# Optimization experiments

Hardware: AMD Instinct MI355X
Metric: run time of the kernel (lower is better)

## Reference

```python
import jax, jax.numpy as jnp
import numpy as np

ALPHA = 1.702
LIMIT = 7.0


def setup_inputs() -> dict:
    key = jax.random.key(0)
    ks = jax.random.split(key, 6)
    A, B, E, M, H = 1, 1, 8, 1024, 2048
    I2 = 4096  # 2 * intermediate_size, interleaved gate/up
    inter = I2 // 2
    return {
        "dispatched": jax.random.normal(ks[0], (A, B, E, M, H), dtype=jnp.float32),
        "w1": jax.random.normal(ks[1], (E, H, I2), dtype=jnp.float32) * 0.02,
        "w1_bias": jax.random.normal(ks[2], (E, I2), dtype=jnp.float32) * 0.02,
        "w2": jax.random.normal(ks[3], (E, inter, H), dtype=jnp.float32) * 0.02,
        "w2_bias": jax.random.normal(ks[4], (E, H), dtype=jnp.float32) * 0.02,
        "sparsity_remap": jax.random.randint(ks[5], (E,), 0, E, dtype=jnp.int32),
        "BD": 1,
        "S": 1024,
    }


def reference(dispatched, w1, w1_bias, w2, w2_bias, sparsity_remap, BD, S):
    # dispatched: [A, B, E, M, H]; w1: [E, H, 2I]; w2: [E, I, H]
    # tt.sparse_matmul == grouped per-expert GEMM; dense math is identical.
    A, Bt, E, M, H = dispatched.shape
    # fused gate+up projection: [A, B, E, M, 2I]
    gu = jnp.einsum("abemh,ehn->abemn", dispatched, w1) + w1_bias[None, None, :, None, :]
    # interleaved gate/up split (gpt_oss activation path)
    gate = gu[..., 0::2]
    up = gu[..., 1::2]
    gate = jnp.minimum(gate, LIMIT)
    up = jnp.clip(up, -LIMIT, LIMIT)
    glu = gate * jax.nn.sigmoid(gate * ALPHA)
    activated = (up + 1.0) * glu  # [A, B, E, M, I]
    inter = activated.shape[-1]
    activated = activated.reshape(A * Bt, E, M, inter)
    # down projection: [A*B, E, M, H]
    down = jnp.einsum("bemi,eih->bemh", activated, w2) + w2_bias[None, :, None, :]
    # permute(1,0,2,3) then untile to [E, 1, BD*S, H]
    out = jnp.transpose(down, (1, 0, 2, 3)).reshape(E, 1, BD * S, H)
    return out
```

## Files before the change

kernel.cpp:

```cpp
#include <hip/hip_runtime.h>
#include <hip/hip_bf16.h>
#include <cstdint>
#include <cstddef>

#define E_ 8
#define M_ 1024
#define H_ 2048
#define I2_ 4096
#define INTER_ 2048

typedef __attribute__((ext_vector_type(8))) __bf16 bf16x8;
typedef __attribute__((ext_vector_type(4))) float f32x4;

__device__ __forceinline__ unsigned short f2bf(float x) {
  union { float f; unsigned u; } v; v.f = x;
  unsigned r = v.u + 0x7fffu + ((v.u >> 16) & 1u);
  return (unsigned short)(r >> 16);
}

__global__ void k_cvt(const float* __restrict__ src, unsigned short* __restrict__ dst, int n4) {
  int i = blockIdx.x * blockDim.x + threadIdx.x;
  int stride = gridDim.x * blockDim.x;
  const float4* s4 = (const float4*)src;
  ushort4* d4 = (ushort4*)dst;
  for (; i < n4; i += stride) {
    float4 v = s4[i];
    ushort4 o;
    o.x = f2bf(v.x); o.y = f2bf(v.y); o.z = f2bf(v.z); o.w = f2bf(v.w);
    d4[i] = o;
  }
}

template<int REMAP>
__global__ __launch_bounds__(1024) void k_transpose(const float* __restrict__ src,
                                                    unsigned short* __restrict__ dst,
                                                    int Ks, int Ns) {
  __shared__ float t[32][65];
  int e = blockIdx.z;
  const float* s = src + (size_t)e * Ks * Ns;
  unsigned short* d = dst + (size_t)e * Ks * Ns;
  int k0 = blockIdx.x * 64;
  int n0 = blockIdx.y * 32;
  int tx = threadIdx.x, ty = threadIdx.y;
  t[tx][ty]      = s[(size_t)(k0 + ty) * Ns + n0 + tx];
  t[tx][ty + 32] = s[(size_t)(k0 + ty + 32) * Ns + n0 + tx];
  __syncthreads();
  int sl = REMAP ? (((ty & 15) << 1) | (ty >> 4)) : ty;
  unsigned short lo = f2bf(t[sl][2 * tx]);
  unsigned short hi = f2bf(t[sl][2 * tx + 1]);
  unsigned v = (unsigned)lo | ((unsigned)hi << 16);
  *(unsigned*)(d + (size_t)(n0 + ty) * Ks + k0 + 2 * tx) = v;
}

template<int ACT, int N, int K>
__global__ __launch_bounds__(256) void k_gemm(
    const unsigned short* __restrict__ A,
    const unsigned short* __restrict__ Bt,
    const float* __restrict__ bias,
    unsigned short* __restrict__ ActOut,
    float* __restrict__ Out)
{
  __shared__ unsigned short la[128 * 64];
  __shared__ unsigned short lb[128 * 64];
  const int tid = threadIdx.x;
  const int lane = tid & 63;
  const int wv = tid >> 6;
  const int wm = wv & 1, wn = wv >> 1;
  const int e = blockIdx.z;
  const int n0 = blockIdx.x * 128;
  const int m0 = blockIdx.y * 128;
  const unsigned short* Ae = A + (size_t)e * M_ * K + (size_t)m0 * K;
  const unsigned short* Be = Bt + (size_t)e * N * K + (size_t)n0 * K;

  const unsigned short* ga[4];
  const unsigned short* gb[4];
  int segb[4];
  #pragma unroll
  for (int t = 0; t < 4; ++t) {
    int s = (wv * 4 + t) * 64 + lane;
    int m = s >> 3;
    int j = (s & 7) ^ (m & 7);
    ga[t] = Ae + (size_t)m * K + j * 8;
    gb[t] = Be + (size_t)m * K + j * 8;
    segb[t] = (wv * 4 + t) * 1024;
  }

  const int c = lane & 15;
  const int q = lane >> 4;

  f32x4 acc[4][4];
  const f32x4 zero = {0.f, 0.f, 0.f, 0.f};
  #pragma unroll
  for (int i = 0; i < 4; ++i)
    #pragma unroll
    for (int j = 0; j < 4; ++j) acc[i][j] = zero;

  const int KT = K / 64;
  for (int kt = 0; kt < KT; ++kt) {
    #pragma unroll
    for (int t = 0; t < 4; ++t) {
      __builtin_amdgcn_global_load_lds(
          (const __attribute__((address_space(1))) void*)(const void*)(ga[t] + kt * 64),
          (__attribute__((address_space(3))) void*)(void*)((char*)la + segb[t]), 16, 0, 0);
      __builtin_amdgcn_global_load_lds(
          (const __attribute__((address_space(1))) void*)(const void*)(gb[t] + kt * 64),
          (__attribute__((address_space(3))) void*)(void*)((char*)lb + segb[t]), 16, 0, 0);
    }
    __syncthreads();
    #pragma unroll
    for (int ks = 0; ks < 2; ++ks) {
      bf16x8 av[4], bv[4];
      #pragma unroll
      for (int mi = 0; mi < 4; ++mi) {
        int row = wm * 64 + mi * 16 + c;
        int slot = row * 8 + ((ks * 4 + q) ^ (c & 7));
        av[mi] = *(const bf16x8*)(la + slot * 8);
      }
      #pragma unroll
      for (int ni = 0; ni < 4; ++ni) {
        int row = wn * 64 + ni * 16 + c;
        int slot = row * 8 + ((ks * 4 + q) ^ (c & 7));
        bv[ni] = *(const bf16x8*)(lb + slot * 8);
      }
      #pragma unroll
      for (int mi = 0; mi < 4; ++mi)
        #pragma unroll
        for (int ni = 0; ni < 4; ++ni)
          acc[mi][ni] = __builtin_amdgcn_mfma_f32_16x16x32_bf16(av[mi], bv[ni], acc[mi][ni], 0, 0, 0);
    }
    __syncthreads();
  }

  if (ACT) {
    unsigned short* ActE = ActOut + (size_t)e * M_ * (N / 2);
    const float* be = bias + (size_t)e * N;
    int colbase = n0 + wn * 64;
    #pragma unroll
    for (int p = 0; p < 2; ++p) {
      int rg = colbase + 32 * p + c;
      int norig = (rg & ~31) | (c << 1);
      float bg = be[norig];
      float bu = be[norig + 1];
      int acol = ((rg >> 5) << 4) + c;
      #pragma unroll
      for (int mi = 0; mi < 4; ++mi) {
        int rowb = m0 + wm * 64 + mi * 16 + q * 4;
        #pragma unroll
        for (int r = 0; r < 4; ++r) {
          float g = acc[mi][2 * p][r] + bg;
          float u = acc[mi][2 * p + 1][r] + bu;
          g = fminf(g, 7.0f);
          u = fminf(fmaxf(u, -7.0f), 7.0f);
          float glu = g / (1.0f + __expf(-1.702f * g));
          float a = (u + 1.0f) * glu;
          ActE[(size_t)(rowb + r) * (N / 2) + acol] = f2bf(a);
        }
      }
    }
  } else {
    float* OutE = Out + (size_t)e * M_ * N;
    const float* be = bias + (size_t)e * N;
    #pragma unroll
    for (int ni = 0; ni < 4; ++ni) {
      int col = n0 + wn * 64 + ni * 16 + c;
      float bb = be[col];
      #pragma unroll
      for (int mi = 0; mi < 4; ++mi) {
        int rowb = m0 + wm * 64 + mi * 16 + q * 4;
        #pragma unroll
        for (int r = 0; r < 4; ++r)
          OutE[(size_t)(rowb + r) * N + col] = acc[mi][ni][r] + bb;
      }
    }
  }
}

__global__ __launch_bounds__(256) void k_naive(const float* __restrict__ disp,
    const float* __restrict__ w1, const float* __restrict__ w1b,
    const float* __restrict__ w2, const float* __restrict__ w2b,
    float* __restrict__ out) {
  __shared__ float xrow[H_];
  __shared__ float act[INTER_];
  int b = blockIdx.x;
  int e = b / M_;
  int m = b % M_;
  const float* x = disp + (size_t)(e * M_ + m) * H_;
  int tid = threadIdx.x;
  for (int k = tid; k < H_; k += 256) xrow[k] = x[k];
  __syncthreads();
  const float* w1e = w1 + (size_t)e * H_ * I2_;
  const float* b1e = w1b + (size_t)e * I2_;
  for (int jj = 0; jj < INTER_ / 256; ++jj) {
    int i = tid + jj * 256;
    float g = b1e[2 * i], u = b1e[2 * i + 1];
    for (int k = 0; k < H_; ++k) {
      float xv = xrow[k];
      g += xv * w1e[(size_t)k * I2_ + 2 * i];
      u += xv * w1e[(size_t)k * I2_ + 2 * i + 1];
    }
    g = fminf(g, 7.0f);
    u = fminf(fmaxf(u, -7.0f), 7.0f);
    float glu = g / (1.0f + __expf(-1.702f * g));
    act[i] = (u + 1.0f) * glu;
  }
  __syncthreads();
  const float* w2e = w2 + (size_t)e * INTER_ * H_;
  const float* b2e = w2b + (size_t)e * H_;
  float* oute = out + (size_t)(e * M_ + m) * H_;
  for (int jj = 0; jj < H_ / 256; ++jj) {
    int h = tid + jj * 256;
    float o = b2e[h];
    for (int i = 0; i < INTER_; ++i) o += act[i] * w2e[(size_t)i * H_ + h];
    oute[h] = o;
  }
}

extern "C" void kernel_launch(void* const* d_in, const int* in_sizes, int n_in,
                              void* d_out, int out_size, void* d_ws, size_t ws_size,
                              hipStream_t stream) {
  const float* disp = (const float*)d_in[0];
  const float* w1   = (const float*)d_in[1];
  const float* w1b  = (const float*)d_in[2];
  const float* w2   = (const float*)d_in[3];
  const float* w2b  = (const float*)d_in[4];
  float* out = (float*)d_out;

  const size_t nA   = (size_t)E_ * M_ * H_;
  const size_t nW1  = (size_t)E_ * H_ * I2_;
  const size_t nW2  = (size_t)E_ * INTER_ * H_;
  const size_t nAct = (size_t)E_ * M_ * INTER_;
  const size_t need = (nA + nW1 + nW2 + nAct) * 2;

  if (ws_size >= need) {
    unsigned short* actb = (unsigned short*)d_ws;
    unsigned short* w1t  = actb + nAct;
    unsigned short* w2t  = w1t + nW1;
    unsigned short* ab   = w2t + nW2;

    k_cvt<<<4096, 256, 0, stream>>>(disp, ab, (int)(nA / 4));
    k_transpose<1><<<dim3(H_ / 64, I2_ / 32, E_), dim3(32, 32), 0, stream>>>(w1, w1t, H_, I2_);
    k_transpose<0><<<dim3(INTER_ / 64, H_ / 32, E_), dim3(32, 32), 0, stream>>>(w2, w2t, INTER_, H_);
    k_gemm<1, I2_, H_><<<dim3(I2_ / 128, M_ / 128, E_), 256, 0, stream>>>(ab, w1t, w1b, actb, nullptr);
    k_gemm<0, H_, INTER_><<<dim3(H_ / 128, M_ / 128, E_), 256, 0, stream>>>(actb, w2t, w2b, nullptr, out);
  } else {
    k_naive<<<E_ * M_, 256, 0, stream>>>(disp, w1, w1b, w2, w2b, out);
  }
}
```

Before: 846.2 us.

## Fuse fp32 weight transpose and bf16 conversion into GEMM B-tile loading

Removes the two separate weight-transpose kernels and has each GEMM block read fp32 weights directly from global memory. It converts them to packed bf16 pairs in registers and stores them into a swizzled LDS layout, with the next tile's loads issued after the barrier to overlap the MFMA work. This avoids writing and re-reading a transposed bf16 weight copy every call. The cost is that each weight tile is now read in fp32 by every M-block, so weight traffic rises, and B fragments are gathered from LDS with scalar 32-bit loads instead of 128-bit vector loads.

```diff
diff --git a/kernel.cpp b/kernel.cpp
--- a/kernel.cpp
+++ b/kernel.cpp
@@ -16,6 +16,16 @@
   union { float f; unsigned u; } v; v.f = x;
   unsigned r = v.u + 0x7fffu + ((v.u >> 16) & 1u);
   return (unsigned short)(r >> 16);
+}
+
+__device__ __forceinline__ unsigned pk2(float lo, float hi) {
+  __hip_bfloat162 h = __float22bfloat162_rn(make_float2(lo, hi));
+  union { __hip_bfloat162 h2; unsigned u; } c; c.h2 = h; return c.u;
+}
+
+__device__ __forceinline__ int bofs(int kp, int r) {
+  int f = (20 * ((kp >> 2) & 3)) ^ ((kp & 1) << 4);
+  return kp * 128 + (r ^ f);
 }
 
 __global__ void k_cvt(const float* __restrict__ src, unsigned short* __restrict__ dst, int n4) {
@@ -31,37 +41,16 @@
   }
 }
 
-template<int REMAP>
-__global__ __launch_bounds__(1024) void k_transpose(const float* __restrict__ src,
-                                                    unsigned short* __restrict__ dst,
-                                                    int Ks, int Ns) {
-  __shared__ float t[32][65];
-  int e = blockIdx.z;
-  const float* s = src + (size_t)e * Ks * Ns;
-  unsigned short* d = dst + (size_t)e * Ks * Ns;
-  int k0 = blockIdx.x * 64;
-  int n0 = blockIdx.y * 32;
-  int tx = threadIdx.x, ty = threadIdx.y;
-  t[tx][ty]      = s[(size_t)(k0 + ty) * Ns + n0 + tx];
-  t[tx][ty + 32] = s[(size_t)(k0 + ty + 32) * Ns + n0 + tx];
-  __syncthreads();
-  int sl = REMAP ? (((ty & 15) << 1) | (ty >> 4)) : ty;
-  unsigned short lo = f2bf(t[sl][2 * tx]);
-  unsigned short hi = f2bf(t[sl][2 * tx + 1]);
-  unsigned v = (unsigned)lo | ((unsigned)hi << 16);
-  *(unsigned*)(d + (size_t)(n0 + ty) * Ks + k0 + 2 * tx) = v;
-}
-
 template<int ACT, int N, int K>
 __global__ __launch_bounds__(256) void k_gemm(
     const unsigned short* __restrict__ A,
-    const unsigned short* __restrict__ Bt,
+    const float* __restrict__ Bf,
     const float* __restrict__ bias,
     unsigned short* __restrict__ ActOut,
     float* __restrict__ Out)
 {
   __shared__ unsigned short la[128 * 64];
-  __shared__ unsigned short lb[128 * 64];
+  __shared__ unsigned lb32[32 * 128];
   const int tid = threadIdx.x;
   const int lane = tid & 63;
   const int wv = tid >> 6;
@@ -70,10 +59,9 @@
   const int n0 = blockIdx.x * 128;
   const int m0 = blockIdx.y * 128;
   const unsigned short* Ae = A + (size_t)e * M_ * K + (size_t)m0 * K;
-  const unsigned short* Be = Bt + (size_t)e * N * K + (size_t)n0 * K;
+  const float* Be = Bf + (size_t)e * K * N + n0;
 
   const unsigned short* ga[4];
-  const unsigned short* gb[4];
   int segb[4];
   #pragma unroll
   for (int t = 0; t < 4; ++t) {
@@ -81,9 +69,21 @@
     int m = s >> 3;
     int j = (s & 7) ^ (m & 7);
     ga[t] = Ae + (size_t)m * K + j * 8;
-    gb[t] = Be + (size_t)m * K + j * 8;
     segb[t] = (wv * 4 + t) * 1024;
   }
+
+  int kpb, colb, rg;
+  if (ACT) {
+    kpb = tid >> 4;
+    int g = tid & 15;
+    colb = 8 * g;
+    rg = 32 * (g >> 2) + 4 * (g & 3);
+  } else {
+    kpb = tid >> 5;
+    colb = 4 * (tid & 31);
+    rg = colb;
+  }
+  const float* bg = Be + (size_t)(2 * kpb) * N + colb;
 
   const int c = lane & 15;
   const int q = lane >> 4;
@@ -95,6 +95,25 @@
     #pragma unroll
     for (int j = 0; j < 4; ++j) acc[i][j] = zero;
 
+  #define LD4(p, off) (*(const float4*)((p) + (off)))
+
+  float4 pb[8];
+  {
+    const float* p = bg;
+    if (ACT) {
+      pb[0] = LD4(p, 0);                    pb[1] = LD4(p, 4);
+      pb[2] = LD4(p, (size_t)N);            pb[3] = LD4(p, (size_t)N + 4);
+      pb[4] = LD4(p, (size_t)32 * N);       pb[5] = LD4(p, (size_t)32 * N + 4);
+      pb[6] = LD4(p, (size_t)33 * N);       pb[7] = LD4(p, (size_t)33 * N + 4);
+    } else {
+      #pragma unroll
+      for (int uu = 0; uu < 4; ++uu) {
+        pb[2 * uu]     = LD4(p, (size_t)(16 * uu) * N);
+        pb[2 * uu + 1] = LD4(p, (size_t)(16 * uu + 1) * N);
+      }
+    }
+  }
+
   const int KT = K / 64;
   for (int kt = 0; kt < KT; ++kt) {
     #pragma unroll
@@ -102,11 +121,46 @@
       __builtin_amdgcn_global_load_lds(
           (const __attribute__((address_space(1))) void*)(const void*)(ga[t] + kt * 64),
           (__attribute__((address_space(3))) void*)(void*)((char*)la + segb[t]), 16, 0, 0);
-      __builtin_amdgcn_global_load_lds(
-          (const __attribute__((address_space(1))) void*)(const void*)(gb[t] + kt * 64),
-          (__attribute__((address_space(3))) void*)(void*)((char*)lb + segb[t]), 16, 0, 0);
+    }
+    if (ACT) {
+      #pragma unroll
+      for (int uu = 0; uu < 2; ++uu) {
+        int kp = kpb + 16 * uu;
+        float4 a0 = pb[4 * uu], a1 = pb[4 * uu + 1], b0 = pb[4 * uu + 2], b1 = pb[4 * uu + 3];
+        uint4 gv, uv;
+        gv.x = pk2(a0.x, b0.x); gv.y = pk2(a0.z, b0.z); gv.z = pk2(a1.x, b1.x); gv.w = pk2(a1.z, b1.z);
+        uv.x = pk2(a0.y, b0.y); uv.y = pk2(a0.w, b0.w); uv.z = pk2(a1.y, b1.y); uv.w = pk2(a1.w, b1.w);
+        *(uint4*)&lb32[bofs(kp, rg)] = gv;
+        *(uint4*)&lb32[bofs(kp, rg + 16)] = uv;
+      }
+    } else {
+      #pragma unroll
+      for (int uu = 0; uu < 4; ++uu) {
+        int kp = kpb + 8 * uu;
+        float4 a = pb[2 * uu], b = pb[2 * uu + 1];
+        uint4 v;
+        v.x = pk2(a.x, b.x); v.y = pk2(a.y, b.y); v.z = pk2(a.z, b.z); v.w = pk2(a.w, b.w);
+        *(uint4*)&lb32[bofs(kp, rg)] = v;
+      }
     }
     __syncthreads();
+
+    if (kt + 1 < KT) {
+      const float* p = bg + (size_t)(kt + 1) * 64 * N;
+      if (ACT) {
+        pb[0] = LD4(p, 0);                    pb[1] = LD4(p, 4);
+        pb[2] = LD4(p, (size_t)N);            pb[3] = LD4(p, (size_t)N + 4);
+        pb[4] = LD4(p, (size_t)32 * N);       pb[5] = LD4(p, (size_t)32 * N + 4);
+        pb[6] = LD4(p, (size_t)33 * N);       pb[7] = LD4(p, (size_t)33 * N + 4);
+      } else {
+        #pragma unroll
+        for (int uu = 0; uu < 4; ++uu) {
+          pb[2 * uu]     = LD4(p, (size_t)(16 * uu) * N);
+          pb[2 * uu + 1] = LD4(p, (size_t)(16 * uu + 1) * N);
+        }
+      }
+    }
+
     #pragma unroll
     for (int ks = 0; ks < 2; ++ks) {
       bf16x8 av[4], bv[4];
@@ -118,9 +172,12 @@
       }
       #pragma unroll
       for (int ni = 0; ni < 4; ++ni) {
-        int row = wn * 64 + ni * 16 + c;
-        int slot = row * 8 + ((ks * 4 + q) ^ (c & 7));
-        bv[ni] = *(const bf16x8*)(lb + slot * 8);
+        int r = wn * 64 + ni * 16 + c;
+        union { unsigned u[4]; bf16x8 v; } t;
+        #pragma unroll
+        for (int jp = 0; jp < 4; ++jp)
+          t.u[jp] = lb32[bofs(ks * 16 + q * 4 + jp, r)];
+        bv[ni] = t.v;
       }
       #pragma unroll
       for (int mi = 0; mi < 4; ++mi)
@@ -130,6 +187,7 @@
     }
     __syncthreads();
   }
+  #undef LD4
 
   if (ACT) {
     unsigned short* ActE = ActOut + (size_t)e * M_ * (N / 2);
@@ -137,18 +195,18 @@
     int colbase = n0 + wn * 64;
     #pragma unroll
     for (int p = 0; p < 2; ++p) {
-      int rg = colbase + 32 * p + c;
-      int norig = (rg & ~31) | (c << 1);
-      float bg = be[norig];
-      float bu = be[norig + 1];
-      int acol = ((rg >> 5) << 4) + c;
+      int rgc = colbase + 32 * p + c;
+      int norig = (rgc & ~31) | (c << 1);
+      float bg_ = be[norig];
+      float bu_ = be[norig + 1];
+      int acol = ((rgc >> 5) << 4) + c;
       #pragma unroll
       for (int mi = 0; mi < 4; ++mi) {
         int rowb = m0 + wm * 64 + mi * 16 + q * 4;
         #pragma unroll
         for (int r = 0; r < 4; ++r) {
-          float g = acc[mi][2 * p][r] + bg;
-          float u = acc[mi][2 * p + 1][r] + bu;
+          float g = acc[mi][2 * p][r] + bg_;
+          float u = acc[mi][2 * p + 1][r] + bu_;
           g = fminf(g, 7.0f);
           u = fminf(fmaxf(u, -7.0f), 7.0f);
           float glu = g / (1.0f + __expf(-1.702f * g));
@@ -226,22 +284,16 @@
   float* out = (float*)d_out;
 
   const size_t nA   = (size_t)E_ * M_ * H_;
-  const size_t nW1  = (size_t)E_ * H_ * I2_;
-  const size_t nW2  = (size_t)E_ * INTER_ * H_;
   const size_t nAct = (size_t)E_ * M_ * INTER_;
-  const size_t need = (nA + nW1 + nW2 + nAct) * 2;
+  const size_t need = (nA + nAct) * 2;
 
   if (ws_size >= need) {
     unsigned short* actb = (unsigned short*)d_ws;
-    unsigned short* w1t  = actb + nAct;
-    unsigned short* w2t  = w1t + nW1;
-    unsigned short* ab   = w2t + nW2;
+    unsigned short* ab   = actb + nAct;
 
     k_cvt<<<4096, 256, 0, stream>>>(disp, ab, (int)(nA / 4));
-    k_transpose<1><<<dim3(H_ / 64, I2_ / 32, E_), dim3(32, 32), 0, stream>>>(w1, w1t, H_, I2_);
-    k_transpose<0><<<dim3(INTER_ / 64, H_ / 32, E_), dim3(32, 32), 0, stream>>>(w2, w2t, INTER_, H_);
-    k_gemm<1, I2_, H_><<<dim3(I2_ / 128, M_ / 128, E_), 256, 0, stream>>>(ab, w1t, w1b, actb, nullptr);
-    k_gemm<0, H_, INTER_><<<dim3(H_ / 128, M_ / 128, E_), 256, 0, stream>>>(actb, w2t, w2b, nullptr, out);
+    k_gemm<1, I2_, H_><<<dim3(I2_ / 128, M_ / 128, E_), 256, 0, stream>>>(ab, w1, w1b, actb, nullptr);
+    k_gemm<0, H_, INTER_><<<dim3(H_ / 128, M_ / 128, E_), 256, 0, stream>>>(actb, w2, w2b, nullptr, out);
   } else {
     k_naive<<<E_ * M_, 256, 0, stream>>>(disp, w1, w1b, w2, w2b, out);
   }
```

Result: faster. 814.3 us (-3.8%).
